# Performance work log

Measured on AMD Instinct MI355X. Metric: run time of the kernel, lower is better.

## Reference

```python
import jax, jax.numpy as jnp
import numpy as np

N = 50000      # nodes
E = 800000     # edges (before self loops)
D = 128        # input_dim == hidden_dim == out_channels
H = 1          # heads
L = 3          # layers
SLOPE = 0.2    # GATv2 leaky_relu negative slope


def setup_inputs() -> dict:
    key = jax.random.key(0)
    ks = jax.random.split(key, 9)
    x = jax.random.normal(ks[0], (N, D), dtype=jnp.float32)
    edge_index = jax.random.randint(ks[1], (2, E), 0, N, dtype=jnp.int32)
    s = 1.0 / np.sqrt(D).astype(np.float32)
    # stacked per-layer GATv2Conv params (all layers are D -> H*D here)
    Wl = jax.random.normal(ks[2], (L, D, H * D), dtype=jnp.float32) * s   # lin_l weights
    bl = jnp.zeros((L, H * D), dtype=jnp.float32)
    Wr = jax.random.normal(ks[3], (L, D, H * D), dtype=jnp.float32) * s   # lin_r weights
    br = jnp.zeros((L, H * D), dtype=jnp.float32)
    att = jax.random.normal(ks[4], (L, H, D), dtype=jnp.float32) * s      # attention vector
    bias = jnp.zeros((L, H * D), dtype=jnp.float32)                       # conv output bias
    return {"x": x, "edge_index": edge_index, "Wl": Wl, "bl": bl,
            "Wr": Wr, "br": br, "att": att, "bias": bias}


def reference(x, edge_index, Wl, bl, Wr, br, att, bias):
    # add self loops (PyG GATv2Conv default)
    loops = jnp.arange(N, dtype=edge_index.dtype)
    src = jnp.concatenate([edge_index[0], loops])  # [E+N] message sources j
    dst = jnp.concatenate([edge_index[1], loops])  # [E+N] message targets i

    h = x
    for l in range(L):
        xl = (h @ Wl[l] + bl[l]).reshape(N, H, D)   # source transform
        xr = (h @ Wr[l] + br[l]).reshape(N, H, D)   # target transform
        # edge-wise GATv2 score: att . leaky_relu(xl_j + xr_i)
        e = jax.nn.leaky_relu(xl[src] + xr[dst], SLOPE)      # [E+N, H, D]
        score = jnp.einsum('ehd,hd->eh', e, att[l])          # [E+N, H]
        # segment softmax over incoming edges of each dst node
        m = jax.ops.segment_max(score, dst, num_segments=N)  # [N, H]
        p = jnp.exp(score - m[dst])
        denom = jax.ops.segment_sum(p, dst, num_segments=N)
        alpha = p / (denom[dst] + 1e-16)                     # [E+N, H]
        # weighted scatter-aggregate of source features
        msg = xl[src] * alpha[:, :, None]                    # [E+N, H, D]
        h = jax.ops.segment_sum(msg, dst, num_segments=N).reshape(N, H * D) + bias[l]
        h = jax.nn.relu(h)
    return jax.nn.log_softmax(h, axis=1)
```

## Files before the change

### kernel.cpp

```cpp
#include <hip/hip_runtime.h>
#include <cstdint>
#include <cstddef>

#define N_NODES 50000
#define N_EDGES 800000
#define ET (N_EDGES + N_NODES)
#define D 128
#define NLAYERS 3
#define LOG2E 1.44269504f
#define DEFER_THR 11.5415603f
#define NB_SCAN ((N_NODES + 1023) / 1024)
#define GEMM_BLOCKS (((N_NODES + 127) / 128) * 2)
#define EDGE_BLOCKS ((ET + 255) / 256)
#define BPAD 136

typedef __bf16 bf16x8 __attribute__((ext_vector_type(8)));
typedef float  f32x4  __attribute__((ext_vector_type(4)));
typedef float  f32x2  __attribute__((ext_vector_type(2)));

__device__ __forceinline__ unsigned short f2bf_rne(float v) {
    unsigned u = __float_as_uint(v);
    u += 0x7fffu + ((u >> 16) & 1u);
    return (unsigned short)(u >> 16);
}
__device__ __forceinline__ f32x2 unpack_bf2(unsigned u) {
    f32x2 r;
    r.x = __uint_as_float(u << 16);
    r.y = __uint_as_float(u & 0xffff0000u);
    return r;
}

__global__ void prep_kernel(const float* __restrict__ x,
                            const float* __restrict__ Wl,
                            const float* __restrict__ Wr,
                            const int* __restrict__ dstp,
                            unsigned short* __restrict__ hhi,
                            unsigned short* __restrict__ wlh,
                            unsigned short* __restrict__ wrh,
                            int* __restrict__ deg)
{
    int idx = blockIdx.x * blockDim.x + threadIdx.x;
    if (idx < (N_NODES * D) / 4) {
        float4 v = ((const float4*)x)[idx];
        uint2 hw;
        hw.x = (unsigned)f2bf_rne(v.x) | ((unsigned)f2bf_rne(v.y) << 16);
        hw.y = (unsigned)f2bf_rne(v.z) | ((unsigned)f2bf_rne(v.w) << 16);
        ((uint2*)hhi)[idx] = hw;
    }
    if (idx < NLAYERS * D * D) {
        int l   = idx / (D * D);
        int rem = idx - l * D * D;
        int kk  = rem / D;
        int nn  = rem - kk * D;
        int tp  = l * D * D + nn * D + kk;
        wlh[tp] = f2bf_rne(Wl[idx]);
        wrh[tp] = f2bf_rne(Wr[idx]);
    }
    if (idx < ET) {
        int dt = (idx < N_EDGES) ? dstp[idx] : idx - N_EDGES;
        atomicAdd(deg + dt, 1);
    }
}

__global__ void scan1_kernel(const int* __restrict__ deg,
                             int* __restrict__ incl, int* __restrict__ bsum)
{
    __shared__ int tmp[1024];
    int tid = threadIdx.x;
    int i = blockIdx.x * 1024 + tid;
    int v = (i < N_NODES) ? deg[i] : 0;
    tmp[tid] = v;
    __syncthreads();
    #pragma unroll
    for (int o = 1; o < 1024; o <<= 1) {
        int t = (tid >= o) ? tmp[tid - o] : 0;
        __syncthreads();
        tmp[tid] += t;
        __syncthreads();
    }
    if (i < N_NODES) incl[i] = tmp[tid];
    if (tid == 1023) bsum[blockIdx.x] = tmp[1023];
}

__global__ void scan3_kernel(const int* __restrict__ deg, const int* __restrict__ incl,
                             const int* __restrict__ bsum,
                             int* __restrict__ off, int* __restrict__ cursor,
                             unsigned short* __restrict__ esrc)
{
    __shared__ int sb[NB_SCAN + 1];
    int tid = threadIdx.x;
    if (tid < 64) {
        int v = (tid < NB_SCAN) ? bsum[tid] : 0;
        int orig = v;
        #pragma unroll
        for (int o = 1; o < 64; o <<= 1) {
            int t = __shfl_up(v, o, 64);
            if (tid >= o) v += t;
        }
        if (tid < NB_SCAN) sb[tid] = v - orig;
        if (tid == 63)     sb[NB_SCAN] = v;
    }
    __syncthreads();
    if (blockIdx.x == 0 && tid < 16) esrc[ET + tid] = 0;
    int i = blockIdx.x * blockDim.x + tid;
    if (i < N_NODES) {
        int e = incl[i] - deg[i] + sb[i >> 10];
        off[i] = e;
        cursor[i] = e;
    } else if (i == N_NODES) {
        off[N_NODES] = sb[NB_SCAN];
    }
}

template <bool WITH_SCATTER>
__global__ __launch_bounds__(256, 4)
void gemm_mfma_kernel(const unsigned short* __restrict__ hhi,
                      const unsigned short* __restrict__ wlh,
                      const unsigned short* __restrict__ wrh,
                      const float* __restrict__ bl, const float* __restrict__ br,
                      const float* __restrict__ att,
                      unsigned short* __restrict__ xlb, unsigned short* __restrict__ xrb,
                      float* __restrict__ bs2,
                      const int* __restrict__ srcp, const int* __restrict__ dstp,
                      int* __restrict__ cursor, unsigned short* __restrict__ esrc, int n)
{
    if (WITH_SCATTER && blockIdx.x >= GEMM_BLOCKS) {
        int e = (blockIdx.x - GEMM_BLOCKS) * 256 + threadIdx.x;
        if (e < ET) {
            int s, dt;
            if (e < N_EDGES) { s = srcp[e]; dt = dstp[e]; }
            else             { s = e - N_EDGES; dt = s; }
            int pos = atomicAdd(cursor + dt, 1);
            esrc[pos] = (unsigned short)s;
        }
        return;
    }

    __shared__ unsigned short lb[64][BPAD];
    __shared__ unsigned short rb[64][BPAD];

    int lane = threadIdx.x & 63;
    int wid  = threadIdx.x >> 6;
    int rowB = blockIdx.x >> 1;
    int half = blockIdx.x & 1;
    int c0   = half * 64;
    int m0   = (rowB * 4 + wid) * 32;
    int gl = lane & 15;
    int kg = lane >> 4;

    {
        const uint4* gl4 = (const uint4*)(wlh + (size_t)c0 * D);
        const uint4* gr4 = (const uint4*)(wrh + (size_t)c0 * D);
        #pragma unroll
        for (int c = 0; c < 4; c++) {
            int idx = c * 256 + threadIdx.x;
            int row = idx >> 4;
            int kc  = idx & 15;
            *(uint4*)&lb[row][kc * 8] = gl4[idx];
            *(uint4*)&rb[row][kc * 8] = gr4[idx];
        }
    }
    __syncthreads();
    if (m0 >= n) return;

    float blc[4], brc[4], attc[4];
    #pragma unroll
    for (int t = 0; t < 4; t++) {
        blc[t]  = bl [c0 + t * 16 + gl];
        brc[t]  = br [c0 + t * 16 + gl];
        attc[t] = att[c0 + t * 16 + gl];
    }

    int ar0 = m0 + gl;      if (ar0 >= n) ar0 = n - 1;
    int ar1 = m0 + 16 + gl; if (ar1 >= n) ar1 = n - 1;
    const unsigned short* ah0 = hhi + (size_t)ar0 * D + kg * 8;
    const unsigned short* ah1 = hhi + (size_t)ar1 * D + kg * 8;

    bf16x8 Ah0[4], Ah1[4];
    #pragma unroll
    for (int ks = 0; ks < 4; ks++) {
        Ah0[ks] = *(const bf16x8*)(ah0 + ks * 32);
        Ah1[ks] = *(const bf16x8*)(ah1 + ks * 32);
    }

    f32x4 accl[2][4], accr[2][4];
    #pragma unroll
    for (int rt = 0; rt < 2; rt++)
        #pragma unroll
        for (int t = 0; t < 4; t++) {
            accl[rt][t] = (f32x4){0.f, 0.f, 0.f, 0.f};
            accr[rt][t] = (f32x4){0.f, 0.f, 0.f, 0.f};
        }

    #pragma unroll
    for (int ks = 0; ks < 4; ks++) {
        #pragma unroll
        for (int t = 0; t < 4; t++) {
            int brow = t * 16 + gl;
            int kofs = kg * 8 + ks * 32;
            bf16x8 bLH = *(const bf16x8*)&lb[brow][kofs];
            bf16x8 bRH = *(const bf16x8*)&rb[brow][kofs];
            accl[0][t] = __builtin_amdgcn_mfma_f32_16x16x32_bf16(Ah0[ks], bLH, accl[0][t], 0, 0, 0);
            accr[0][t] = __builtin_amdgcn_mfma_f32_16x16x32_bf16(Ah0[ks], bRH, accr[0][t], 0, 0, 0);
            accl[1][t] = __builtin_amdgcn_mfma_f32_16x16x32_bf16(Ah1[ks], bLH, accl[1][t], 0, 0, 0);
            accr[1][t] = __builtin_amdgcn_mfma_f32_16x16x32_bf16(Ah1[ks], bRH, accr[1][t], 0, 0, 0);
        }
    }

    #pragma unroll
    for (int rt = 0; rt < 2; rt++) {
        #pragma unroll
        for (int r = 0; r < 4; r++) {
            int row = m0 + rt * 16 + kg * 4 + r;
            if (row < n) {
                float p = 0.f;
                #pragma unroll
                for (int t = 0; t < 4; t++) {
                    int col = c0 + t * 16 + gl;
                    float vl = accl[rt][t][r] + blc[t];
                    xlb[(size_t)row * D + col] = f2bf_rne(vl);
                    xrb[(size_t)row * D + col] = f2bf_rne(accr[rt][t][r] + brc[t]);
                    p = fmaf(attc[t], vl, p);
                }
                p += __shfl_xor(p, 1, 64);
                p += __shfl_xor(p, 2, 64);
                p += __shfl_xor(p, 4, 64);
                p += __shfl_xor(p, 8, 64);
                if (gl == 0) bs2[row * 2 + half] = 0.6f * LOG2E * p;
            }
        }
    }
}

template <int LAST>
__global__ void node_attn_kernel(const unsigned short* __restrict__ xlb,
                                 const unsigned short* __restrict__ xrb,
                                 const float* __restrict__ bs2,
                                 const float* __restrict__ att,
                                 const float* __restrict__ bias,
                                 const int* __restrict__ off,
                                 const unsigned short* __restrict__ esrc,
                                 float* __restrict__ outF,
                                 unsigned short* __restrict__ hhi)
{
    int i    = (int)((blockIdx.x * (size_t)blockDim.x + threadIdx.x) >> 6);
    int lane = threadIdx.x & 63;
    if (i >= N_NODES) return;
    int g  = lane >> 4;
    int gl = lane & 15;
    int fb = gl * 8;

    float aav[8];
    f32x2 rr2[4];
    {
        float4 a0 = *(const float4*)(att + fb);
        float4 a1 = *(const float4*)(att + fb + 4);
        const float s = 0.4f * LOG2E;
        aav[0] = s * a0.x; aav[1] = s * a0.y; aav[2] = s * a0.z; aav[3] = s * a0.w;
        aav[4] = s * a1.x; aav[5] = s * a1.y; aav[6] = s * a1.z; aav[7] = s * a1.w;
        uint4 r4 = *(const uint4*)(xrb + (size_t)i * D + fb);
        rr2[0] = unpack_bf2(r4.x); rr2[1] = unpack_bf2(r4.y);
        rr2[2] = unpack_bf2(r4.z); rr2[3] = unpack_bf2(r4.w);
    }

    float m = -1e30f, l = 0.f;
    f32x2 acc2[4];
    #pragma unroll
    for (int j = 0; j < 4; j++) acc2[j] = (f32x2){0.f, 0.f};

    int k    = off[i];
    int kEnd = off[i + 1];

    int ka = k + g, kb = k + 4 + g;
    bool va = ka < kEnd, vb = kb < kEnd;
    int sa = esrc[ka];
    int sb = esrc[kb];
    uint4 x4a = *(const uint4*)(xlb + (size_t)sa * D + fb);
    uint4 x4b = *(const uint4*)(xlb + (size_t)sb * D + fb);
    float2 ba2 = *(const float2*)(bs2 + sa * 2);
    float2 bb2 = *(const float2*)(bs2 + sb * 2);
    float bsa = ba2.x + ba2.y, bsb = bb2.x + bb2.y;

    while (k < kEnd) {
        int kn = k + 8;
        uint4 nxa = x4a, nxb = x4b;
        float nbsa = bsa, nbsb = bsb;
        bool nva = false, nvb = false;
        if (kn < kEnd) {
            int nka = kn + g, nkb = kn + 4 + g;
            nva = nka < kEnd; nvb = nkb < kEnd;
            int nsa = esrc[nka];
            int nsb = esrc[nkb];
            nxa = *(const uint4*)(xlb + (size_t)nsa * D + fb);
            nxb = *(const uint4*)(xlb + (size_t)nsb * D + fb);
            float2 na2 = *(const float2*)(bs2 + nsa * 2);
            float2 nb2 = *(const float2*)(bs2 + nsb * 2);
            nbsa = na2.x + na2.y; nbsb = nb2.x + nb2.y;
        }
        f32x2 xa2[4], xb2[4];
        xa2[0] = unpack_bf2(x4a.x); xa2[1] = unpack_bf2(x4a.y);
        xa2[2] = unpack_bf2(x4a.z); xa2[3] = unpack_bf2(x4a.w);
        xb2[0] = unpack_bf2(x4b.x); xb2[1] = unpack_bf2(x4b.y);
        xb2[2] = unpack_bf2(x4b.z); xb2[3] = unpack_bf2(x4b.w);

        float s2a = 0.f, s2b = 0.f;
        #pragma unroll
        for (int q = 0; q < 4; q++) {
            f32x2 ta = xa2[q] + rr2[q];
            f32x2 tb = xb2[q] + rr2[q];
            s2a = fmaf(aav[2*q],   fabsf(ta.x), s2a);
            s2a = fmaf(aav[2*q+1], fabsf(ta.y), s2a);
            s2b = fmaf(aav[2*q],   fabsf(tb.x), s2b);
            s2b = fmaf(aav[2*q+1], fabsf(tb.y), s2b);
        }
        s2a += __shfl_xor(s2a, 1, 64);
        s2b += __shfl_xor(s2b, 1, 64);
        s2a += __shfl_xor(s2a, 2, 64);
        s2b += __shfl_xor(s2b, 2, 64);
        s2a += __shfl_xor(s2a, 4, 64);
        s2b += __shfl_xor(s2b, 4, 64);
        s2a += __shfl_xor(s2a, 8, 64);
        s2b += __shfl_xor(s2b, 8, 64);
        float sca = bsa + s2a;
        float scb = bsb + s2b;
        float mx2 = fmaxf(sca, scb);
        if (__any(mx2 > m + DEFER_THR)) {
            float mn = fmaxf(m, mx2);
            float f  = exp2f(m - mn);
            float pa = va ? exp2f(sca - mn) : 0.f;
            float pb = vb ? exp2f(scb - mn) : 0.f;
            l = l * f + pa + pb;
            f32x2 fv = {f, f}, pa2 = {pa, pa}, pb2 = {pb, pb};
            #pragma unroll
            for (int q = 0; q < 4; q++)
                acc2[q] = __builtin_elementwise_fma(acc2[q], fv,
                          __builtin_elementwise_fma(xa2[q], pa2, xb2[q] * pb2));
            m = mn;
        } else {
            float pa = va ? exp2f(sca - m) : 0.f;
            float pb = vb ? exp2f(scb - m) : 0.f;
            l += pa + pb;
            f32x2 pa2 = {pa, pa}, pb2 = {pb, pb};
            #pragma unroll
            for (int q = 0; q < 4; q++)
                acc2[q] = __builtin_elementwise_fma(xa2[q], pa2,
                          __builtin_elementwise_fma(xb2[q], pb2, acc2[q]));
        }
        x4a = nxa; x4b = nxb; bsa = nbsa; bsb = nbsb; va = nva; vb = nvb;
        k = kn;
    }

    #pragma unroll
    for (int o = 16; o <= 32; o <<= 1) {
        float mo  = __shfl_xor(m, o, 64);
        float lo2 = __shfl_xor(l, o, 64);
        float mn  = fmaxf(m, mo);
        float f1  = exp2f(m - mn);
        float f2s = exp2f(mo - mn);
        l = l * f1 + lo2 * f2s;
        f32x2 f1v = {f1, f1}, f2v = {f2s, f2s};
        #pragma unroll
        for (int q = 0; q < 4; q++) {
            f32x2 ao;
            ao.x = __shfl_xor(acc2[q].x, o, 64);
            ao.y = __shfl_xor(acc2[q].y, o, 64);
            acc2[q] = __builtin_elementwise_fma(acc2[q], f1v, ao * f2v);
        }
        m = mn;
    }

    float inv = 1.f / (l + 1e-16f);
    float hv[8];
    {
        float4 b0 = *(const float4*)(bias + fb);
        float4 b1 = *(const float4*)(bias + fb + 4);
        float bb[8] = {b0.x, b0.y, b0.z, b0.w, b1.x, b1.y, b1.z, b1.w};
        #pragma unroll
        for (int q = 0; q < 4; q++) {
            hv[2*q]   = fmaxf(fmaf(acc2[q].x, inv, bb[2*q]),   0.f);
            hv[2*q+1] = fmaxf(fmaf(acc2[q].y, inv, bb[2*q+1]), 0.f);
        }
    }

    if (LAST) {
        float mx = hv[0];
        #pragma unroll
        for (int j = 1; j < 8; j++) mx = fmaxf(mx, hv[j]);
        mx = fmaxf(mx, __shfl_xor(mx, 1, 64));
        mx = fmaxf(mx, __shfl_xor(mx, 2, 64));
        mx = fmaxf(mx, __shfl_xor(mx, 4, 64));
        mx = fmaxf(mx, __shfl_xor(mx, 8, 64));
        float se = 0.f;
        #pragma unroll
        for (int j = 0; j < 8; j++) se += __expf(hv[j] - mx);
        se += __shfl_xor(se, 1, 64);
        se += __shfl_xor(se, 2, 64);
        se += __shfl_xor(se, 4, 64);
        se += __shfl_xor(se, 8, 64);
        float ls = logf(se) + mx;
        if (g == 0) {
            float4 o0 = make_float4(hv[0] - ls, hv[1] - ls, hv[2] - ls, hv[3] - ls);
            float4 o1 = make_float4(hv[4] - ls, hv[5] - ls, hv[6] - ls, hv[7] - ls);
            float* dst = outF + (size_t)i * D + fb;
            *(float4*)(dst)     = o0;
            *(float4*)(dst + 4) = o1;
        }
    } else {
        if (g == 0) {
            unsigned pk[4];
            #pragma unroll
            for (int j = 0; j < 4; j++) {
                pk[j] = (unsigned)f2bf_rne(hv[j * 2]) |
                        ((unsigned)f2bf_rne(hv[j * 2 + 1]) << 16);
            }
            unsigned short* dst = hhi + (size_t)i * D + fb;
            *(uint4*)dst = make_uint4(pk[0], pk[1], pk[2], pk[3]);
        }
    }
}

extern "C" void kernel_launch(void* const* d_in, const int* in_sizes, int n_in,
                              void* d_out, int out_size, void* d_ws, size_t ws_size,
                              hipStream_t stream)
{
    const float* x    = (const float*)d_in[0];
    const int*   ei   = (const int*)  d_in[1];
    const float* Wl   = (const float*)d_in[2];
    const float* bl   = (const float*)d_in[3];
    const float* Wr   = (const float*)d_in[4];
    const float* br   = (const float*)d_in[5];
    const float* att  = (const float*)d_in[6];
    const float* bias = (const float*)d_in[7];
    float* out = (float*)d_out;

    const int* srcp = ei;
    const int* dstp = ei + N_EDGES;

    const size_t ND = (size_t)N_NODES * D;
    const size_t WSZ = (size_t)NLAYERS * D * D;
    char* ws = (char*)d_ws;
    unsigned short* xlb = (unsigned short*)ws; ws += ND * sizeof(unsigned short);
    unsigned short* xrb = (unsigned short*)ws; ws += ND * sizeof(unsigned short);
    unsigned short* hhi = (unsigned short*)ws; ws += ND * sizeof(unsigned short);
    unsigned short* wlh = (unsigned short*)ws; ws += WSZ * sizeof(unsigned short);
    unsigned short* wrh = (unsigned short*)ws; ws += WSZ * sizeof(unsigned short);
    float* bs2  = (float*)ws; ws += (size_t)N_NODES * 2 * sizeof(float);
    int* deg    = (int*)ws;  ws += (size_t)N_NODES * sizeof(int);
    int* incl   = (int*)ws;  ws += (size_t)N_NODES * sizeof(int);
    int* off    = (int*)ws;  ws += (size_t)(N_NODES + 1) * sizeof(int);
    int* cursor = (int*)ws;  ws += (size_t)N_NODES * sizeof(int);
    int* bsum   = (int*)ws;  ws += (size_t)NB_SCAN * sizeof(int);
    unsigned short* esrc = (unsigned short*)ws; ws += ((size_t)ET + 16) * sizeof(unsigned short);

    const int prepGrid  = (int)((ND / 4 + 255) / 256);
    const int nodeGrid  = (N_NODES + 3) / 4;
    const int scan3Grid = (N_NODES + 1 + 255) / 256;

    hipMemsetAsync(deg, 0, (size_t)N_NODES * sizeof(int), stream);
    prep_kernel<<<prepGrid, 256, 0, stream>>>(x, Wl, Wr, dstp, hhi, wlh, wrh, deg);

    scan1_kernel<<<NB_SCAN, 1024, 0, stream>>>(deg, incl, bsum);
    scan3_kernel<<<scan3Grid, 256, 0, stream>>>(deg, incl, bsum, off, cursor, esrc);

    for (int l = 0; l < NLAYERS; l++) {
        size_t wOff = (size_t)l * D * D;
        if (l == 0) {
            gemm_mfma_kernel<true><<<GEMM_BLOCKS + EDGE_BLOCKS, 256, 0, stream>>>(
                hhi, wlh + wOff, wrh + wOff,
                bl + (size_t)l * D, br + (size_t)l * D, att + (size_t)l * D,
                xlb, xrb, bs2, srcp, dstp, cursor, esrc, N_NODES);
        } else {
            gemm_mfma_kernel<false><<<GEMM_BLOCKS, 256, 0, stream>>>(
                hhi, wlh + wOff, wrh + wOff,
                bl + (size_t)l * D, br + (size_t)l * D, att + (size_t)l * D,
                xlb, xrb, bs2, nullptr, nullptr, nullptr, nullptr, N_NODES);
        }

        if (l == NLAYERS - 1) {
            node_attn_kernel<1><<<nodeGrid, 256, 0, stream>>>(
                xlb, xrb, bs2, att + (size_t)l * D, bias + (size_t)l * D,
                off, esrc, out, nullptr);
        } else {
            node_attn_kernel<0><<<nodeGrid, 256, 0, stream>>>(
                xlb, xrb, bs2, att + (size_t)l * D, bias + (size_t)l * D,
                off, esrc, nullptr, hhi);
        }
    }
}
```

Baseline: 307.5 us.

## Stage GEMM outputs through LDS for coalesced stores; fold edge scatter into GEMM blocks

The GEMM epilogue now writes bf16 results into shared memory and then issues coalesced 16-byte row stores to xl/xr, replacing scattered 2-byte global writes. The CSR edge scatter no longer uses separate extra blocks. Each GEMM thread prefetches five edges before the GEMM and does the atomic scatter after the epilogue, which overlaps the edge loads with compute and shrinks the grid. The cost is extra register pressure from holding the edge indices, plus one more barrier.

```diff
diff --git a/kernel.cpp b/kernel.cpp
--- a/kernel.cpp
+++ b/kernel.cpp
@@ -11,8 +11,10 @@
 #define DEFER_THR 11.5415603f
 #define NB_SCAN ((N_NODES + 1023) / 1024)
 #define GEMM_BLOCKS (((N_NODES + 127) / 128) * 2)
-#define EDGE_BLOCKS ((ET + 255) / 256)
+#define SCAT_STRIDE (GEMM_BLOCKS * 256)
+#define EPT 5
 #define BPAD 136
+#define OPAD 68
 
 typedef __bf16 bf16x8 __attribute__((ext_vector_type(8)));
 typedef float  f32x4  __attribute__((ext_vector_type(4)));
@@ -124,36 +126,37 @@
                       const int* __restrict__ srcp, const int* __restrict__ dstp,
                       int* __restrict__ cursor, unsigned short* __restrict__ esrc, int n)
 {
-    if (WITH_SCATTER && blockIdx.x >= GEMM_BLOCKS) {
-        int e = (blockIdx.x - GEMM_BLOCKS) * 256 + threadIdx.x;
-        if (e < ET) {
-            int s, dt;
-            if (e < N_EDGES) { s = srcp[e]; dt = dstp[e]; }
-            else             { s = e - N_EDGES; dt = s; }
-            int pos = atomicAdd(cursor + dt, 1);
-            esrc[pos] = (unsigned short)s;
-        }
-        return;
-    }
-
-    __shared__ unsigned short lb[64][BPAD];
-    __shared__ unsigned short rb[64][BPAD];
-
-    int lane = threadIdx.x & 63;
-    int wid  = threadIdx.x >> 6;
+    __shared__ unsigned short sm[2 * 64 * BPAD];
+    unsigned short (*lb)[BPAD] = (unsigned short(*)[BPAD])sm;
+    unsigned short (*rb)[BPAD] = (unsigned short(*)[BPAD])(sm + 64 * BPAD);
+
+    int tid  = threadIdx.x;
+    int lane = tid & 63;
+    int wid  = tid >> 6;
     int rowB = blockIdx.x >> 1;
     int half = blockIdx.x & 1;
     int c0   = half * 64;
-    int m0   = (rowB * 4 + wid) * 32;
+    int m0   = rowB * 128 + wid * 32;
     int gl = lane & 15;
     int kg = lane >> 4;
+
+    int es[EPT], ed[EPT];
+    if (WITH_SCATTER) {
+        #pragma unroll
+        for (int j = 0; j < EPT; j++) {
+            int e = blockIdx.x * 256 + tid + j * SCAT_STRIDE;
+            if (e < N_EDGES)      { es[j] = srcp[e]; ed[j] = dstp[e]; }
+            else if (e < ET)      { es[j] = e - N_EDGES; ed[j] = es[j]; }
+            else                  { es[j] = -1; ed[j] = -1; }
+        }
+    }
 
     {
         const uint4* gl4 = (const uint4*)(wlh + (size_t)c0 * D);
         const uint4* gr4 = (const uint4*)(wrh + (size_t)c0 * D);
         #pragma unroll
         for (int c = 0; c < 4; c++) {
-            int idx = c * 256 + threadIdx.x;
+            int idx = c * 256 + tid;
             int row = idx >> 4;
             int kc  = idx & 15;
             *(uint4*)&lb[row][kc * 8] = gl4[idx];
@@ -161,7 +164,6 @@
         }
     }
     __syncthreads();
-    if (m0 >= n) return;
 
     float blc[4], brc[4], attc[4];
     #pragma unroll
@@ -207,26 +209,51 @@
         }
     }
 
+    __syncthreads();
+    unsigned short (*obL)[OPAD] = (unsigned short(*)[OPAD])sm;
+    unsigned short (*obR)[OPAD] = (unsigned short(*)[OPAD])(sm + 128 * OPAD);
+
     #pragma unroll
     for (int rt = 0; rt < 2; rt++) {
         #pragma unroll
         for (int r = 0; r < 4; r++) {
-            int row = m0 + rt * 16 + kg * 4 + r;
-            if (row < n) {
-                float p = 0.f;
-                #pragma unroll
-                for (int t = 0; t < 4; t++) {
-                    int col = c0 + t * 16 + gl;
-                    float vl = accl[rt][t][r] + blc[t];
-                    xlb[(size_t)row * D + col] = f2bf_rne(vl);
-                    xrb[(size_t)row * D + col] = f2bf_rne(accr[rt][t][r] + brc[t]);
-                    p = fmaf(attc[t], vl, p);
-                }
-                p += __shfl_xor(p, 1, 64);
-                p += __shfl_xor(p, 2, 64);
-                p += __shfl_xor(p, 4, 64);
-                p += __shfl_xor(p, 8, 64);
-                if (gl == 0) bs2[row * 2 + half] = 0.6f * LOG2E * p;
+            int lrow = wid * 32 + rt * 16 + kg * 4 + r;
+            int grow = rowB * 128 + lrow;
+            float p = 0.f;
+            #pragma unroll
+            for (int t = 0; t < 4; t++) {
+                float vl = accl[rt][t][r] + blc[t];
+                obL[lrow][t * 16 + gl] = f2bf_rne(vl);
+                obR[lrow][t * 16 + gl] = f2bf_rne(accr[rt][t][r] + brc[t]);
+                p = fmaf(attc[t], vl, p);
+            }
+            p += __shfl_xor(p, 1, 64);
+            p += __shfl_xor(p, 2, 64);
+            p += __shfl_xor(p, 4, 64);
+            p += __shfl_xor(p, 8, 64);
+            if (gl == 0 && grow < n) bs2[grow * 2 + half] = 0.6f * LOG2E * p;
+        }
+    }
+    __syncthreads();
+
+    #pragma unroll
+    for (int c = 0; c < 4; c++) {
+        int idx  = c * 256 + tid;
+        int lrow = idx >> 3;
+        int kc   = idx & 7;
+        int grow = rowB * 128 + lrow;
+        if (grow < n) {
+            *(uint4*)(xlb + (size_t)grow * D + c0 + kc * 8) = *(const uint4*)&obL[lrow][kc * 8];
+            *(uint4*)(xrb + (size_t)grow * D + c0 + kc * 8) = *(const uint4*)&obR[lrow][kc * 8];
+        }
+    }
+
+    if (WITH_SCATTER) {
+        #pragma unroll
+        for (int j = 0; j < EPT; j++) {
+            if (ed[j] >= 0) {
+                int pos = atomicAdd(cursor + ed[j], 1);
+                esrc[pos] = (unsigned short)es[j];
             }
         }
     }
@@ -465,7 +492,7 @@
     for (int l = 0; l < NLAYERS; l++) {
         size_t wOff = (size_t)l * D * D;
         if (l == 0) {
-            gemm_mfma_kernel<true><<<GEMM_BLOCKS + EDGE_BLOCKS, 256, 0, stream>>>(
+            gemm_mfma_kernel<true><<<GEMM_BLOCKS, 256, 0, stream>>>(
                 hhi, wlh + wOff, wrh + wOff,
                 bl + (size_t)l * D, br + (size_t)l * D, att + (size_t)l * D,
                 xlb, xrb, bs2, srcp, dstp, cursor, esrc, N_NODES);
```

Measured after the change: 313.9 us. +2.1%, slower.
